# Optimization experiments

Measured on AMD Instinct MI355X. Metric: run time of the kernel, lower is better.

## Reference

```python
import jax, jax.numpy as jnp
import numpy as np

B, T, A, H, E = 512, 64, 32, 512, 32


def sinusoidal_pos_encoding(t, dim):
    # t: (B, T) float positions -> (B, T, dim)
    half = dim // 2
    freqs = jnp.exp(-jnp.log(10000.0) * jnp.arange(half, dtype=jnp.float32) / half)
    ang = t[..., None] * freqs  # (B, T, half)
    return jnp.concatenate([jnp.sin(ang), jnp.cos(ang)], axis=-1)


def cat_linear(x, W, b, cat_ids):
    # x: (B, T, Din); W: (E, Din, Dout); b: (E, Dout); cat_ids: (B,)
    Wg = W[cat_ids]            # (B, Din, Dout) gathered per-sample weights
    bg = b[cat_ids][:, None]   # (B, 1, Dout)
    return jnp.einsum('btd,bdh->bth', x, Wg) + bg


def swish(x):
    return x * jax.nn.sigmoid(x)


def setup_inputs() -> dict:
    key = jax.random.key(0)
    ks = jax.random.split(key, 10)
    s = lambda fan_in: 1.0 / np.sqrt(fan_in)
    return {
        'actions': jax.random.normal(ks[0], (B, T, A), dtype=jnp.float32),
        'timesteps': jax.random.uniform(ks[1], (B,), dtype=jnp.float32),
        'cat_ids': jax.random.randint(ks[2], (B,), 0, E),
        'W1': jax.random.normal(ks[3], (E, A, H), dtype=jnp.float32) * s(A),
        'b1': jnp.zeros((E, H), dtype=jnp.float32),
        'W2': jax.random.normal(ks[4], (E, 2 * H, H), dtype=jnp.float32) * s(2 * H),
        'b2': jnp.zeros((E, H), dtype=jnp.float32),
        'W3': jax.random.normal(ks[5], (E, H, H), dtype=jnp.float32) * s(H),
        'b3': jnp.zeros((E, H), dtype=jnp.float32),
    }


def reference(actions, timesteps, cat_ids, W1, b1, W2, b2, W3, b3):
    b, t, _ = actions.shape
    timesteps_bt = jnp.broadcast_to(timesteps[:, None], (b, t))
    a_emb = cat_linear(actions, W1, b1, cat_ids)              # (B, T, H)
    tau_emb = sinusoidal_pos_encoding(timesteps_bt, H).astype(a_emb.dtype)
    x = jnp.concatenate([a_emb, tau_emb], axis=-1)            # (B, T, 2H)
    x = swish(cat_linear(x, W2, b2, cat_ids))                 # (B, T, H)
    x = cat_linear(x, W3, b3, cat_ids)                        # (B, T, H)
    return x
```

## Files before the change

### kernel.cpp

```cpp
#include <hip/hip_runtime.h>
#include <hip/hip_bf16.h>

#define B_ 512
#define T_ 64
#define A_ 32
#define H_ 512
#define E_ 32
#define MAX_TASKS 272
#define CAP_ 168
#define GRID_ (8 * CAP_)
#define TSC 16

typedef unsigned short u16;
typedef unsigned int u32;
typedef __attribute__((ext_vector_type(8))) short short8;
typedef __attribute__((ext_vector_type(4))) float floatx4;

static __device__ __forceinline__ u16 f2bf(float f) {
    u32 u = __builtin_bit_cast(u32, f);
    u += 0x7fffu + ((u >> 16) & 1u);
    return (u16)(u >> 16);
}

static __device__ __forceinline__ void gl2lds16(const u16* g, u16* l) {
    __builtin_amdgcn_global_load_lds(
        (const __attribute__((address_space(1))) void*)g,
        (__attribute__((address_space(3))) void*)l, 16, 0, 0);
}

__global__ void group_kernel(const int* __restrict__ cat_ids,
                             int* __restrict__ sample_list,
                             int4* __restrict__ tasks,
                             int* __restrict__ itemlist,
                             int* __restrict__ eoff_g,
                             int* __restrict__ ecnt_g) {
    __shared__ int cnt[E_], off[E_], cur[E_], toff[E_], jc[8];
    __shared__ int total, fb;
    int tid = threadIdx.x;
    if (tid < E_) { cnt[tid] = 0; cur[tid] = 0; }
    __syncthreads();
    int e = cat_ids[tid];
    atomicAdd(&cnt[e], 1);
    __syncthreads();
    if (tid == 0) {
        int run = 0, trun = 0;
        for (int i = 0; i < E_; i++) {
            off[i] = run;  run += cnt[i];
            toff[i] = trun; trun += (cnt[i] + 1) >> 1;
        }
        total = trun;
    }
    __syncthreads();
    if (tid < E_) {
        int c = cnt[tid], o = off[tid], to = toff[tid];
        eoff_g[tid] = o;
        ecnt_g[tid] = c;
        for (int j = 0; j < c; j += 2)
            tasks[to++] = make_int4(tid, o + j, (c - j >= 2) ? 2 : 1, 0);
    }
    if (tid < 8) {
        int J = 0;
        for (int cc = 0; cc < 4; cc++) J += 4 * ((cnt[tid + 8 * cc] + 1) >> 1);
        jc[tid] = J;
    }
    __syncthreads();
    if (tid == 0) {
        int f = 0;
        for (int x = 0; x < 8; x++) if (jc[x] > CAP_) f = 1;
        fb = f;
    }
    __syncthreads();
    if (!fb) {
        if (tid < 8) {
            int j = 0;
            for (int cc = 0; cc < 4; cc++) {
                int ee = tid + 8 * cc;
                int nt = (cnt[ee] + 1) >> 1, t0 = toff[ee];
                for (int t = t0; t < t0 + nt; t++)
                    for (int nb = 0; nb < 4; nb++) {
                        itemlist[tid + 8 * j] = (t << 2) | nb;
                        j++;
                    }
            }
            for (; j < CAP_; j++) itemlist[tid + 8 * j] = -1;
        }
    } else {
        for (int f = tid; f < GRID_; f += 512)
            itemlist[f] = (f < 4 * total) ? f : -1;
    }
    int p = atomicAdd(&cur[e], 1);
    sample_list[off[e] + p] = tid;
}

__global__ __launch_bounds__(256) void embed_kernel(
        const float* __restrict__ actions, const float* __restrict__ timesteps,
        const int* __restrict__ cat_ids, const float* __restrict__ W1,
        const float* __restrict__ b1, const float* __restrict__ b2,
        u16* __restrict__ a_emb, float* __restrict__ tauG,
        float* __restrict__ bias2s) {
    int b = blockIdx.x;
    int tid = threadIdx.x;
    int e = cat_ids[b];

    {
        float tval = timesteps[b];
        float freq = expf(-9.210340371976184f * (float)tid * (1.0f / 256.0f));
        float ang = tval * freq;
        tauG[(size_t)b * H_ + tid]       = sinf(ang);
        tauG[(size_t)b * H_ + 256 + tid] = cosf(ang);
        bias2s[(size_t)b * H_ + tid]       = b2[e * H_ + tid];
        bias2s[(size_t)b * H_ + 256 + tid] = b2[e * H_ + 256 + tid];
    }

    __shared__ float act[T_ * A_];
    const float* asrc = actions + (size_t)b * T_ * A_;
    for (int i = tid; i < T_ * A_; i += 256) act[i] = asrc[i];
    __syncthreads();

    const float* w1 = W1 + (size_t)e * A_ * H_;
    int n0 = tid, n1 = tid + 256;
    float wA[A_], wB[A_];
#pragma unroll
    for (int k = 0; k < A_; k++) {
        wA[k] = w1[k * H_ + n0];
        wB[k] = w1[k * H_ + n1];
    }
    float bA = b1[e * H_ + n0], bB = b1[e * H_ + n1];
    u16* orow = a_emb + (size_t)b * T_ * H_;
    for (int tt = 0; tt < T_; tt++) {
        float accA = bA, accB = bB;
#pragma unroll
        for (int k = 0; k < A_; k++) {
            float a = act[tt * A_ + k];
            accA = fmaf(a, wA[k], accA);
            accB = fmaf(a, wB[k], accB);
        }
        orow[tt * H_ + n0] = f2bf(accA);
        orow[tt * H_ + n1] = f2bf(accB);
    }
}

__global__ __launch_bounds__(256) void convert_transpose(
        const float* __restrict__ W, u16* __restrict__ Wt, int srcK, int dstK) {
    int n = blockIdx.y * 256 + threadIdx.x;
    int k0 = blockIdx.x * 64;
    int e = blockIdx.z;
    const float* src = W + ((size_t)e * srcK + k0) * H_ + n;
    short8 out[8];
#pragma unroll
    for (int j = 0; j < 64; j++)
        out[j >> 3][j & 7] = (short)f2bf(src[(size_t)j * H_]);
    u16* dst = Wt + ((size_t)e * H_ + n) * dstK + k0;
#pragma unroll
    for (int c = 0; c < 8; c++) *(short8*)(dst + c * 8) = out[c];
}

__global__ __launch_bounds__(256) void tau_bias_kernel(
        const float* __restrict__ W2, const float* __restrict__ tauG,
        const int* __restrict__ sample_list,
        const int* __restrict__ eoff, const int* __restrict__ ecnt,
        float* __restrict__ bias2s) {
    int cc = blockIdx.x;
    int e  = blockIdx.y;
    int kq = blockIdx.z;
    int cnt = ecnt[e], off = eoff[e];
    if (cnt == 0) return;
    int tid = threadIdx.x;
    int ks = tid >> 6;
    int ln = tid & 63;
    int n = cc * 64 + ln;
    const float* wb = W2 + ((size_t)e * 1024 + 512 + kq * 128) * H_;

    __shared__ float tauT[128][20];
    __shared__ float pS[4][TSC][64];

    for (int c0 = 0; c0 < cnt; c0 += TSC) {
        for (int i = tid; i < TSC * 128; i += 256) {
            int sl = i >> 7, k = i & 127;
            float v = 0.f;
            if (c0 + sl < cnt)
                v = tauG[(size_t)sample_list[off + c0 + sl] * H_ + kq * 128 + k];
            tauT[k][sl] = v;
        }
        __syncthreads();

        float a[TSC];
#pragma unroll
        for (int s = 0; s < TSC; s++) a[s] = 0.f;

#pragma unroll 8
        for (int j = 0; j < 32; j++) {
            int k = ks * 32 + j;
            float w = wb[(size_t)k * H_ + n];
            float tv[TSC];
            *(float4*)&tv[0]  = *(const float4*)&tauT[k][0];
            *(float4*)&tv[4]  = *(const float4*)&tauT[k][4];
            *(float4*)&tv[8]  = *(const float4*)&tauT[k][8];
            *(float4*)&tv[12] = *(const float4*)&tauT[k][12];
#pragma unroll
            for (int s = 0; s < TSC; s++) a[s] = fmaf(tv[s], w, a[s]);
        }

#pragma unroll
        for (int s = 0; s < TSC; s++) pS[ks][s][ln] = a[s];
        __syncthreads();

        for (int o = tid; o < TSC * 64; o += 256) {
            int sl = o >> 6, l = o & 63;
            if (c0 + sl < cnt) {
                float v = pS[0][sl][l] + pS[1][sl][l] +
                          pS[2][sl][l] + pS[3][sl][l];
                int s = sample_list[off + c0 + sl];
                unsafeAtomicAdd(&bias2s[(size_t)s * H_ + cc * 64 + l], v);
            }
        }
        __syncthreads();
    }
}

template <int DIN, bool PSBIAS, bool DO_SWISH, bool OUT_BF16>
__global__ __launch_bounds__(256, 2) void moe_gemm(
        const u16* __restrict__ xsrc, const u16* __restrict__ Wt,
        const float* __restrict__ bias,
        const int* __restrict__ sample_list, const int4* __restrict__ tasks,
        const int* __restrict__ itemlist, void* __restrict__ outp) {
    int item = itemlist[blockIdx.x];
    if (item < 0) return;
    int4 task = tasks[item >> 2];
    int nb = item & 3;
    int ns = task.z;
    int e = task.x;
    int s0 = sample_list[task.y];
    int s1 = (ns > 1) ? sample_list[task.y + 1] : s0;
    int n0 = nb * 128;

    int tid = threadIdx.x;
    int lane = tid & 63, wv = tid >> 6;
    int wr = wv >> 1, wc = wv & 1;
    int quad = lane >> 4, c15 = lane & 15;
    int r8 = lane >> 3, cg = lane & 7;

    __shared__ __align__(16) u16 xs[2][128 * 64];
    __shared__ __align__(16) u16 wt[2][128 * 64];

    floatx4 acc[4][4];
    floatx4 zero4 = {0.f, 0.f, 0.f, 0.f};
#pragma unroll
    for (int i = 0; i < 4; i++)
#pragma unroll
        for (int j = 0; j < 4; j++) acc[i][j] = zero4;

    const u16* wbase = Wt + (size_t)(e * H_ + n0) * DIN;
    int kc_sw = (cg ^ r8) * 8;

    auto stage = [&](int b, int k0) {
#pragma unroll
        for (int h = 0; h < 4; h++) {
            int rbase = h * 32 + wv * 8;
            int s = (h < 2) ? s0 : s1;
            int t = (rbase + r8) & 63;
            gl2lds16(xsrc + ((size_t)s * T_ + t) * H_ + k0 + kc_sw,
                     &xs[b][rbase * 64]);
        }
#pragma unroll
        for (int h = 0; h < 4; h++) {
            int nbase = h * 32 + wv * 8;
            gl2lds16(wbase + (size_t)(nbase + r8) * DIN + k0 + kc_sw,
                     &wt[b][nbase * 64]);
        }
    };

    auto compute = [&](int b) {
#pragma unroll
        for (int kk = 0; kk < 2; kk++) {
            int c = kk * 4 + quad;
            short8 af[4], bfr[4];
#pragma unroll
            for (int i = 0; i < 4; i++) {
                int row = wr * 64 + i * 16 + c15;
                af[i] = *(const short8*)&xs[b][row * 64 + ((c ^ (row & 7)) * 8)];
                int nr = wc * 64 + i * 16 + c15;
                bfr[i] = *(const short8*)&wt[b][nr * 64 + ((c ^ (nr & 7)) * 8)];
            }
#pragma unroll
            for (int mt = 0; mt < 4; mt++)
#pragma unroll
                for (int nt = 0; nt < 4; nt++)
                    acc[mt][nt] = __builtin_amdgcn_mfma_f32_16x16x32_bf16(
                            af[mt], bfr[nt], acc[mt][nt], 0, 0, 0);
        }
    };

    constexpr int KI = DIN / 64;
    stage(0, 0);
    __syncthreads();
#pragma unroll
    for (int t = 0; t < KI; ++t) {
        if (t + 1 < KI) stage((t + 1) & 1, (t + 1) * 64);
        compute(t & 1);
        if (t + 1 < KI) __syncthreads();
    }

    if (wr >= ns) return;
    int s = (wr == 0) ? s0 : s1;
    const float* bp = PSBIAS ? (bias + (size_t)s * H_)
                             : (bias + (size_t)e * H_);
#pragma unroll
    for (int mt = 0; mt < 4; mt++) {
        int tb = mt * 16 + quad * 4;
#pragma unroll
        for (int nt = 0; nt < 4; nt++) {
            int col = n0 + wc * 64 + nt * 16 + c15;
            float bv = bp[col];
#pragma unroll
            for (int r = 0; r < 4; r++) {
                float v = acc[mt][nt][r] + bv;
                if (DO_SWISH) v = v / (1.0f + expf(-v));
                size_t oidx = ((size_t)s * T_ + tb + r) * H_ + col;
                if (OUT_BF16) ((u16*)outp)[oidx] = f2bf(v);
                else          ((float*)outp)[oidx] = v;
            }
        }
    }
}

extern "C" void kernel_launch(void* const* d_in, const int* in_sizes, int n_in,
                              void* d_out, int out_size, void* d_ws, size_t ws_size,
                              hipStream_t stream) {
    const float* actions   = (const float*)d_in[0];
    const float* timesteps = (const float*)d_in[1];
    const int*   cat_ids   = (const int*)d_in[2];
    const float* W1 = (const float*)d_in[3];
    const float* b1 = (const float*)d_in[4];
    const float* W2 = (const float*)d_in[5];
    const float* b2 = (const float*)d_in[6];
    const float* W3 = (const float*)d_in[7];
    const float* b3 = (const float*)d_in[8];

    char* ws = (char*)d_ws;
    u16* a_emb = (u16*)ws;
    u16* y     = (u16*)(ws + (size_t)32 * 1024 * 1024);
    char* meta = ws + (size_t)64 * 1024 * 1024 + 512 * 1024;
    int*  sample_list = (int*)meta;
    int4* tasks       = (int4*)(meta + 8192);
    int*  itemlist    = (int*)(meta + 16384);
    int*  eoff        = (int*)(meta + 24576);
    int*  ecnt        = (int*)(meta + 24576 + 128);
    u16*  Wt2a   = (u16*)d_out;
    float* bias2s = (float*)((char*)d_out + (size_t)48 * 1024 * 1024);
    float* tauG   = (float*)((char*)d_out + (size_t)52 * 1024 * 1024);
    u16*  Wt3    = a_emb;

    hipLaunchKernelGGL(group_kernel, dim3(1), dim3(512), 0, stream,
                       cat_ids, sample_list, tasks, itemlist, eoff, ecnt);
    hipLaunchKernelGGL(embed_kernel, dim3(512), dim3(256), 0, stream,
                       actions, timesteps, cat_ids, W1, b1, b2, a_emb, tauG,
                       bias2s);
    hipLaunchKernelGGL(convert_transpose, dim3(H_ / 64, 2, E_), dim3(256),
                       0, stream, W2, Wt2a, 2 * H_, H_);
    hipLaunchKernelGGL(tau_bias_kernel, dim3(8, E_, 4), dim3(256), 0, stream,
                       W2, tauG, sample_list, eoff, ecnt, bias2s);
    hipLaunchKernelGGL((moe_gemm<H_, true, true, true>), dim3(GRID_),
                       dim3(256), 0, stream,
                       a_emb, Wt2a, bias2s, sample_list, tasks, itemlist,
                       (void*)y);
    hipLaunchKernelGGL(convert_transpose, dim3(H_ / 64, 2, E_), dim3(256),
                       0, stream, W3, Wt3, H_, H_);
    hipLaunchKernelGGL((moe_gemm<H_, false, false, false>), dim3(GRID_),
                       dim3(256), 0, stream,
                       y, Wt3, b3, sample_list, tasks, itemlist, d_out);
}
```

Measured before the change: 303.3 us.

## Fuse setup kernels and deepen GEMM prefetch to two stages in flight

Merges the grouping kernel into the embed kernel as an extra block, and merges the W2 convert-transpose with the tau-bias kernel into one prep launch, cutting launch count and serial dependencies. The embed kernel now uses 512 threads with one output column each. The MoE GEMM main loop now issues loads for the next two K tiles ahead, using explicit vmcnt waits and raw barriers, so memory latency overlaps more with MFMA compute. The hand-written waitcnt counts depend on how many loads each stage issues and could race if that assumption is wrong. The embed kernel's higher register use per block could also cut occupancy.

```diff
diff --git a/kernel.cpp b/kernel.cpp
--- a/kernel.cpp
+++ b/kernel.cpp
@@ -28,123 +28,111 @@
         (__attribute__((address_space(3))) void*)l, 16, 0, 0);
 }
 
-__global__ void group_kernel(const int* __restrict__ cat_ids,
-                             int* __restrict__ sample_list,
-                             int4* __restrict__ tasks,
-                             int* __restrict__ itemlist,
-                             int* __restrict__ eoff_g,
-                             int* __restrict__ ecnt_g) {
-    __shared__ int cnt[E_], off[E_], cur[E_], toff[E_], jc[8];
-    __shared__ int total, fb;
-    int tid = threadIdx.x;
-    if (tid < E_) { cnt[tid] = 0; cur[tid] = 0; }
-    __syncthreads();
-    int e = cat_ids[tid];
-    atomicAdd(&cnt[e], 1);
-    __syncthreads();
-    if (tid == 0) {
-        int run = 0, trun = 0;
-        for (int i = 0; i < E_; i++) {
-            off[i] = run;  run += cnt[i];
-            toff[i] = trun; trun += (cnt[i] + 1) >> 1;
-        }
-        total = trun;
-    }
-    __syncthreads();
-    if (tid < E_) {
-        int c = cnt[tid], o = off[tid], to = toff[tid];
-        eoff_g[tid] = o;
-        ecnt_g[tid] = c;
-        for (int j = 0; j < c; j += 2)
-            tasks[to++] = make_int4(tid, o + j, (c - j >= 2) ? 2 : 1, 0);
-    }
-    if (tid < 8) {
-        int J = 0;
-        for (int cc = 0; cc < 4; cc++) J += 4 * ((cnt[tid + 8 * cc] + 1) >> 1);
-        jc[tid] = J;
-    }
-    __syncthreads();
-    if (tid == 0) {
-        int f = 0;
-        for (int x = 0; x < 8; x++) if (jc[x] > CAP_) f = 1;
-        fb = f;
-    }
-    __syncthreads();
-    if (!fb) {
-        if (tid < 8) {
-            int j = 0;
-            for (int cc = 0; cc < 4; cc++) {
-                int ee = tid + 8 * cc;
-                int nt = (cnt[ee] + 1) >> 1, t0 = toff[ee];
-                for (int t = t0; t < t0 + nt; t++)
-                    for (int nb = 0; nb < 4; nb++) {
-                        itemlist[tid + 8 * j] = (t << 2) | nb;
-                        j++;
-                    }
-            }
-            for (; j < CAP_; j++) itemlist[tid + 8 * j] = -1;
-        }
-    } else {
-        for (int f = tid; f < GRID_; f += 512)
-            itemlist[f] = (f < 4 * total) ? f : -1;
-    }
-    int p = atomicAdd(&cur[e], 1);
-    sample_list[off[e] + p] = tid;
-}
-
-__global__ __launch_bounds__(256) void embed_kernel(
+__global__ __launch_bounds__(512) void embed_group_kernel(
         const float* __restrict__ actions, const float* __restrict__ timesteps,
         const int* __restrict__ cat_ids, const float* __restrict__ W1,
         const float* __restrict__ b1, const float* __restrict__ b2,
         u16* __restrict__ a_emb, float* __restrict__ tauG,
-        float* __restrict__ bias2s) {
+        float* __restrict__ bias2s,
+        int* __restrict__ sample_list, int4* __restrict__ tasks,
+        int* __restrict__ itemlist, int* __restrict__ eoff_g,
+        int* __restrict__ ecnt_g) {
+    int tid = threadIdx.x;
+
+    if (blockIdx.x == B_) {
+        __shared__ int cnt[E_], off[E_], cur[E_], toff[E_], jc[8];
+        __shared__ int total, fb;
+        if (tid < E_) { cnt[tid] = 0; cur[tid] = 0; }
+        __syncthreads();
+        int e = cat_ids[tid];
+        atomicAdd(&cnt[e], 1);
+        __syncthreads();
+        if (tid == 0) {
+            int run = 0, trun = 0;
+            for (int i = 0; i < E_; i++) {
+                off[i] = run;  run += cnt[i];
+                toff[i] = trun; trun += (cnt[i] + 1) >> 1;
+            }
+            total = trun;
+        }
+        __syncthreads();
+        if (tid < E_) {
+            int c = cnt[tid], o = off[tid], to = toff[tid];
+            eoff_g[tid] = o;
+            ecnt_g[tid] = c;
+            for (int j = 0; j < c; j += 2)
+                tasks[to++] = make_int4(tid, o + j, (c - j >= 2) ? 2 : 1, 0);
+        }
+        if (tid < 8) {
+            int J = 0;
+            for (int cc = 0; cc < 4; cc++)
+                J += 4 * ((cnt[tid + 8 * cc] + 1) >> 1);
+            jc[tid] = J;
+        }
+        __syncthreads();
+        if (tid == 0) {
+            int f = 0;
+            for (int x = 0; x < 8; x++) if (jc[x] > CAP_) f = 1;
+            fb = f;
+        }
+        __syncthreads();
+        if (!fb) {
+            if (tid < 8) {
+                int j = 0;
+                for (int cc = 0; cc < 4; cc++) {
+                    int ee = tid + 8 * cc;
+                    int nt = (cnt[ee] + 1) >> 1, t0 = toff[ee];
+                    for (int t = t0; t < t0 + nt; t++)
+                        for (int nb = 0; nb < 4; nb++) {
+                            itemlist[tid + 8 * j] = (t << 2) | nb;
+                            j++;
+                        }
+                }
+                for (; j < CAP_; j++) itemlist[tid + 8 * j] = -1;
+            }
+        } else {
+            for (int f = tid; f < GRID_; f += 512)
+                itemlist[f] = (f < 4 * total) ? f : -1;
+        }
+        int p = atomicAdd(&cur[e], 1);
+        sample_list[off[e] + p] = tid;
+        return;
+    }
+
     int b = blockIdx.x;
-    int tid = threadIdx.x;
     int e = cat_ids[b];
-
     {
         float tval = timesteps[b];
-        float freq = expf(-9.210340371976184f * (float)tid * (1.0f / 256.0f));
+        int kk = tid & 255;
+        float freq = expf(-9.210340371976184f * (float)kk * (1.0f / 256.0f));
         float ang = tval * freq;
-        tauG[(size_t)b * H_ + tid]       = sinf(ang);
-        tauG[(size_t)b * H_ + 256 + tid] = cosf(ang);
-        bias2s[(size_t)b * H_ + tid]       = b2[e * H_ + tid];
-        bias2s[(size_t)b * H_ + 256 + tid] = b2[e * H_ + 256 + tid];
+        tauG[(size_t)b * H_ + tid] = (tid < 256) ? sinf(ang) : cosf(ang);
+        bias2s[(size_t)b * H_ + tid] = b2[e * H_ + tid];
     }
 
     __shared__ float act[T_ * A_];
     const float* asrc = actions + (size_t)b * T_ * A_;
-    for (int i = tid; i < T_ * A_; i += 256) act[i] = asrc[i];
+    for (int i = tid; i < T_ * A_; i += 512) act[i] = asrc[i];
     __syncthreads();
 
     const float* w1 = W1 + (size_t)e * A_ * H_;
-    int n0 = tid, n1 = tid + 256;
-    float wA[A_], wB[A_];
-#pragma unroll
-    for (int k = 0; k < A_; k++) {
-        wA[k] = w1[k * H_ + n0];
-        wB[k] = w1[k * H_ + n1];
-    }
-    float bA = b1[e * H_ + n0], bB = b1[e * H_ + n1];
+    float wcol[A_];
+#pragma unroll
+    for (int k = 0; k < A_; k++) wcol[k] = w1[k * H_ + tid];
+    float bb = b1[e * H_ + tid];
     u16* orow = a_emb + (size_t)b * T_ * H_;
     for (int tt = 0; tt < T_; tt++) {
-        float accA = bA, accB = bB;
-#pragma unroll
-        for (int k = 0; k < A_; k++) {
-            float a = act[tt * A_ + k];
-            accA = fmaf(a, wA[k], accA);
-            accB = fmaf(a, wB[k], accB);
-        }
-        orow[tt * H_ + n0] = f2bf(accA);
-        orow[tt * H_ + n1] = f2bf(accB);
-    }
-}
-
-__global__ __launch_bounds__(256) void convert_transpose(
-        const float* __restrict__ W, u16* __restrict__ Wt, int srcK, int dstK) {
-    int n = blockIdx.y * 256 + threadIdx.x;
-    int k0 = blockIdx.x * 64;
-    int e = blockIdx.z;
+        float acc = bb;
+#pragma unroll
+        for (int k = 0; k < A_; k++)
+            acc = fmaf(act[tt * A_ + k], wcol[k], acc);
+        orow[tt * H_ + tid] = f2bf(acc);
+    }
+}
+
+static __device__ __forceinline__ void ct_block(
+        const float* __restrict__ W, u16* __restrict__ Wt,
+        int srcK, int dstK, int e, int k0, int n) {
     const float* src = W + ((size_t)e * srcK + k0) * H_ + n;
     short8 out[8];
 #pragma unroll
@@ -155,24 +143,40 @@
     for (int c = 0; c < 8; c++) *(short8*)(dst + c * 8) = out[c];
 }
 
-__global__ __launch_bounds__(256) void tau_bias_kernel(
-        const float* __restrict__ W2, const float* __restrict__ tauG,
-        const int* __restrict__ sample_list,
+__global__ __launch_bounds__(256) void convert_transpose(
+        const float* __restrict__ W, u16* __restrict__ Wt, int srcK, int dstK) {
+    ct_block(W, Wt, srcK, dstK, blockIdx.z, blockIdx.x * 64,
+             blockIdx.y * 256 + threadIdx.x);
+}
+
+__global__ __launch_bounds__(256) void prep_kernel(
+        const float* __restrict__ W2, u16* __restrict__ Wt2a,
+        const float* __restrict__ tauG, const int* __restrict__ sample_list,
         const int* __restrict__ eoff, const int* __restrict__ ecnt,
         float* __restrict__ bias2s) {
-    int cc = blockIdx.x;
-    int e  = blockIdx.y;
-    int kq = blockIdx.z;
+    int tid = threadIdx.x;
+    int bid = blockIdx.x;
+
+    __shared__ float tauT[128][20];
+    __shared__ float pS[4][TSC][64];
+
+    if (bid < 512) {
+        int e = bid >> 4, sub = bid & 15;
+        ct_block(W2, Wt2a, 2 * H_, H_, e, (sub & 7) * 64,
+                 (sub >> 3) * 256 + tid);
+        return;
+    }
+
+    int id = bid - 512;
+    int cc = id & 7;
+    int e  = (id >> 3) & 31;
+    int kq = id >> 8;
     int cnt = ecnt[e], off = eoff[e];
     if (cnt == 0) return;
-    int tid = threadIdx.x;
     int ks = tid >> 6;
     int ln = tid & 63;
     int n = cc * 64 + ln;
     const float* wb = W2 + ((size_t)e * 1024 + 512 + kq * 128) * H_;
-
-    __shared__ float tauT[128][20];
-    __shared__ float pS[4][TSC][64];
 
     for (int c0 = 0; c0 < cnt; c0 += TSC) {
         for (int i = tid; i < TSC * 128; i += 256) {
@@ -293,12 +297,25 @@
 
     constexpr int KI = DIN / 64;
     stage(0, 0);
-    __syncthreads();
+    stage(1, 64);
+    asm volatile("s_waitcnt vmcnt(8)" ::: "memory");
+    __builtin_amdgcn_s_barrier();
+    __builtin_amdgcn_sched_barrier(0);
 #pragma unroll
     for (int t = 0; t < KI; ++t) {
-        if (t + 1 < KI) stage((t + 1) & 1, (t + 1) * 64);
         compute(t & 1);
-        if (t + 1 < KI) __syncthreads();
+        if (t + 1 < KI) {
+            __builtin_amdgcn_s_barrier();
+            __builtin_amdgcn_sched_barrier(0);
+            if (t + 2 < KI) {
+                stage(t & 1, (t + 2) * 64);
+                asm volatile("s_waitcnt vmcnt(8)" ::: "memory");
+            } else {
+                asm volatile("s_waitcnt vmcnt(0)" ::: "memory");
+            }
+            __builtin_amdgcn_s_barrier();
+            __builtin_amdgcn_sched_barrier(0);
+        }
     }
 
     if (wr >= ns) return;
@@ -351,15 +368,12 @@
     float* tauG   = (float*)((char*)d_out + (size_t)52 * 1024 * 1024);
     u16*  Wt3    = a_emb;
 
-    hipLaunchKernelGGL(group_kernel, dim3(1), dim3(512), 0, stream,
-                       cat_ids, sample_list, tasks, itemlist, eoff, ecnt);
-    hipLaunchKernelGGL(embed_kernel, dim3(512), dim3(256), 0, stream,
-                       actions, timesteps, cat_ids, W1, b1, b2, a_emb, tauG,
-                       bias2s);
-    hipLaunchKernelGGL(convert_transpose, dim3(H_ / 64, 2, E_), dim3(256),
-                       0, stream, W2, Wt2a, 2 * H_, H_);
-    hipLaunchKernelGGL(tau_bias_kernel, dim3(8, E_, 4), dim3(256), 0, stream,
-                       W2, tauG, sample_list, eoff, ecnt, bias2s);
+    hipLaunchKernelGGL(embed_group_kernel, dim3(B_ + 1), dim3(512), 0, stream,
+                       actions, timesteps, cat_ids, W1, b1, b2,
+                       a_emb, tauG, bias2s,
+                       sample_list, tasks, itemlist, eoff, ecnt);
+    hipLaunchKernelGGL(prep_kernel, dim3(1536), dim3(256), 0, stream,
+                       W2, Wt2a, tauG, sample_list, eoff, ecnt, bias2s);
     hipLaunchKernelGGL((moe_gemm<H_, true, true, true>), dim3(GRID_),
                        dim3(256), 0, stream,
                        a_emb, Wt2a, bias2s, sample_list, tasks, itemlist,
```

Result: faster. 285.1 us (-6.0%).
